# Kernel tuning notes

Measured on AMD Instinct MI355X. Metric: run time of the kernel, lower is better.

## Reference

```python
import jax, jax.numpy as jnp
import numpy as np

TOKENS, IN_F, OUT_F = 8192, 4096, 4096

def setup_inputs() -> dict:
    key = jax.random.key(0)
    k1, k2, k3, k4 = jax.random.split(key, 4)
    x = jax.random.randint(k1, (TOKENS, IN_F), -128, 128, dtype=jnp.int32).astype(jnp.int8)
    weight = jax.random.randint(k2, (OUT_F, IN_F), -128, 128, dtype=jnp.int32).astype(jnp.int8)
    # per-output-channel static dequant scale (small positive values, as for int8 quant)
    dequant_scale = (jax.random.uniform(k3, (OUT_F,), dtype=jnp.float32) * 0.01 + 1e-4)
    bias = (jax.random.normal(k4, (OUT_F,), dtype=jnp.float32) * 0.02).astype(jnp.float16)
    return {"x": x, "weight": weight, "dequant_scale": dequant_scale, "bias": bias}

def reference(x, weight, dequant_scale, bias):
    acc = jnp.matmul(x.astype(jnp.int32), weight.T.astype(jnp.int32))
    # fused epilogue: per-channel dequant + bias add, cast to fp16 output
    out = (acc.astype(jnp.float32) * dequant_scale[None, :]
           + bias.astype(jnp.float32)[None, :]).astype(jnp.float16)
    # module's forward returns (output, bias)
    return (out, bias)
```

## Files before the change

### kernel.cpp

```cpp
#include <hip/hip_runtime.h>
#include <hip/hip_fp16.h>

#define TOKENS 8192
#define IN_F   4096
#define OUT_F  4096
#define NKT    (IN_F / 64)

typedef __attribute__((ext_vector_type(4))) int i32x4;

__global__ void prep_kernel(const int4* __restrict__ xs, const int4* __restrict__ ws,
                            const float* __restrict__ bias,
                            int4* __restrict__ xp, int4* __restrict__ wp,
                            float* __restrict__ out_tail) {
    const int NX = TOKENS * IN_F / 16;
    const int NW = OUT_F * IN_F / 16;
    const int gid = blockIdx.x * blockDim.x + threadIdx.x;
    const int stride = gridDim.x * blockDim.x;
    for (int i = gid; i < NX + NW; i += stride) {
        const int4* s; int4* d; int j;
        if (i < NX) { s = xs; d = xp; j = i; }
        else        { s = ws; d = wp; j = i - NX; }
        int4 a = s[4 * j + 0];
        int4 b = s[4 * j + 1];
        int4 c = s[4 * j + 2];
        int4 e = s[4 * j + 3];
        int4 o;
        o.x = (int)((a.x & 0xffu) | ((a.y & 0xffu) << 8) | ((a.z & 0xffu) << 16) | ((a.w & 0xffu) << 24));
        o.y = (int)((b.x & 0xffu) | ((b.y & 0xffu) << 8) | ((b.z & 0xffu) << 16) | ((b.w & 0xffu) << 24));
        o.z = (int)((c.x & 0xffu) | ((c.y & 0xffu) << 8) | ((c.z & 0xffu) << 16) | ((c.w & 0xffu) << 24));
        o.w = (int)((e.x & 0xffu) | ((e.y & 0xffu) << 8) | ((e.z & 0xffu) << 16) | ((e.w & 0xffu) << 24));
        d[j] = o;
    }
    if (gid < OUT_F) out_tail[gid] = bias[gid];
}

__global__ __launch_bounds__(512, 2) void gemm_i8_kernel(
    const char* __restrict__ A,
    const char* __restrict__ B,
    const float* __restrict__ scale,
    const float* __restrict__ bias,
    float* __restrict__ out)
{
    __shared__ char lds[4][2][16384];

    const int tid  = threadIdx.x;
    const int wid  = tid >> 6;
    const int lane = tid & 63;
    const int wm   = wid >> 2;
    const int wn   = wid & 3;

    const int nwg = gridDim.x;
    const int bid = blockIdx.x;
    const int swz = (bid & 7) * (nwg >> 3) + (bid >> 3);
    const int tm = swz >> 4;
    const int tn = swz & 15;

    const char* ag = A + (size_t)(tm * 256) * IN_F;
    const char* bg = B + (size_t)(tn * 256) * IN_F;

    const int srow16 = wid * 16 + (lane >> 2);
    const int schunk = ((lane & 3) ^ ((lane >> 2) & 3)) << 4;
    const int ldst   = wid * 1024 + lane * 16;

    i32x4 acc[8][4];
#pragma unroll
    for (int m = 0; m < 8; ++m)
#pragma unroll
        for (int n = 0; n < 4; ++n)
            acc[m][n] = (i32x4){0, 0, 0, 0};

#define STAGE(r, t)                                                                        \
    do {                                                                                   \
        _Pragma("unroll")                                                                  \
        for (int j = 0; j < 2; ++j) {                                                      \
            size_t go = (size_t)(j * 128 + srow16) * IN_F + (size_t)(t) * 64 + schunk;     \
            __builtin_amdgcn_global_load_lds(                                              \
                (const __attribute__((address_space(1))) void*)(ag + go),                  \
                (__attribute__((address_space(3))) void*)(&lds[r][0][j * 8192 + ldst]),    \
                16, 0, 0);                                                                 \
            __builtin_amdgcn_global_load_lds(                                              \
                (const __attribute__((address_space(1))) void*)(bg + go),                  \
                (__attribute__((address_space(3))) void*)(&lds[r][1][j * 8192 + ldst]),    \
                16, 0, 0);                                                                 \
        }                                                                                  \
    } while (0)

    const int kg   = lane >> 4;
    const int sxa  = lane & 3;
    const int aoff = (wm * 128 + (lane & 15)) * 64 + ((kg ^ sxa) << 4);
    const int boff = (wn * 64  + (lane & 15)) * 64 + ((kg ^ sxa) << 4);

#define STEP(t, VM, DOSTAGE)                                                               \
    do {                                                                                   \
        asm volatile("s_waitcnt vmcnt(" #VM ")" ::: "memory");                             \
        __builtin_amdgcn_s_barrier();                                                      \
        asm volatile("" ::: "memory");                                                     \
        __builtin_amdgcn_sched_barrier(0);                                                 \
        if (DOSTAGE) STAGE(((t) + 3) & 3, (t) + 3);                                        \
        const char* al = &lds[(t) & 3][0][0];                                              \
        const char* bl = &lds[(t) & 3][1][0];                                              \
        i32x4 afr[8], bfr[4];                                                              \
        _Pragma("unroll")                                                                  \
        for (int m = 0; m < 8; ++m) afr[m] = *(const i32x4*)(al + aoff + m * 1024);        \
        _Pragma("unroll")                                                                  \
        for (int n = 0; n < 4; ++n) bfr[n] = *(const i32x4*)(bl + boff + n * 1024);        \
        __builtin_amdgcn_s_setprio(1);                                                     \
        _Pragma("unroll")                                                                  \
        for (int m = 0; m < 8; ++m)                                                        \
            _Pragma("unroll")                                                              \
            for (int n = 0; n < 4; ++n)                                                    \
                acc[m][n] = __builtin_amdgcn_mfma_i32_16x16x64_i8(                         \
                    afr[m], bfr[n], acc[m][n], 0, 0, 0);                                   \
        __builtin_amdgcn_s_setprio(0);                                                     \
    } while (0)

    STAGE(0, 0);
    STAGE(1, 1);
    STAGE(2, 2);

    for (int t = 0; t < NKT - 3; ++t) STEP(t, 8, 1);
    STEP(NKT - 3, 8, 0);
    STEP(NKT - 2, 4, 0);
    STEP(NKT - 1, 0, 0);

    const int col  = tn * 256 + wn * 64 + (lane & 15);
    const int row0 = tm * 256 + wm * 128 + ((lane >> 4) << 2);
    float sc[4], bi[4];
#pragma unroll
    for (int n = 0; n < 4; ++n) {
        sc[n] = scale[col + n * 16];
        bi[n] = bias[col + n * 16];
    }
#pragma unroll
    for (int m = 0; m < 8; ++m)
#pragma unroll
        for (int n = 0; n < 4; ++n)
#pragma unroll
            for (int r = 0; r < 4; ++r) {
                float v = (float)acc[m][n][r] * sc[n] + bi[n];
                out[(size_t)(row0 + m * 16 + r) * OUT_F + col + n * 16] =
                    (float)__float2half_rn(v);
            }
#undef STAGE
#undef STEP
}

extern "C" void kernel_launch(void* const* d_in, const int* in_sizes, int n_in,
                              void* d_out, int out_size, void* d_ws, size_t ws_size,
                              hipStream_t stream) {
    const int*   x_i32 = (const int*)d_in[0];
    const int*   w_i32 = (const int*)d_in[1];
    const float* scale = (const float*)d_in[2];
    const float* bias  = (const float*)d_in[3];
    float*       out   = (float*)d_out;

    char* xp = (char*)d_ws;
    char* wp = xp + (size_t)TOKENS * IN_F;

    prep_kernel<<<3072, 256, 0, stream>>>((const int4*)x_i32, (const int4*)w_i32, bias,
                                          (int4*)xp, (int4*)wp, out + (size_t)TOKENS * OUT_F);

    gemm_i8_kernel<<<(TOKENS / 256) * (OUT_F / 256), 512, 0, stream>>>(xp, wp, scale, bias, out);
}
```

Measured before the change: 192.0 us.

## Switch GEMM to 128x256 tiles with K=128 triple-buffered two-phase pipeline

The block tile shrinks from 256x256 to 128x256 while the K step grows from 64 to 128, and the LDS ring goes from four buffers to three. Each K tile is split into two phases, and the async global-to-LDS loads for tile t+2 are interleaved into those phases with explicit vmcnt waits and extra barriers. The grid doubles and per-thread accumulators halve, which should improve occupancy and load balance. In exchange, arithmetic intensity per block drops and more barriers are taken per K step.

```diff
diff --git a/kernel.cpp b/kernel.cpp
--- a/kernel.cpp
+++ b/kernel.cpp
@@ -4,8 +4,11 @@
 #define TOKENS 8192
 #define IN_F   4096
 #define OUT_F  4096
-#define NKT    (IN_F / 64)
+#define NKT    (IN_F / 128)
 
+#define ABYTES 16384
+#define BBYTES 32768
+#define BUFSZ  (ABYTES + BBYTES)
 typedef __attribute__((ext_vector_type(4))) int i32x4;
 
 __global__ void prep_kernel(const int4* __restrict__ xs, const int4* __restrict__ ws,
@@ -41,7 +44,7 @@
     const float* __restrict__ bias,
     float* __restrict__ out)
 {
-    __shared__ char lds[4][2][16384];
+    __shared__ char lds[3 * BUFSZ];
 
     const int tid  = threadIdx.x;
     const int wid  = tid >> 6;
@@ -55,76 +58,98 @@
     const int tm = swz >> 4;
     const int tn = swz & 15;
 
-    const char* ag = A + (size_t)(tm * 256) * IN_F;
+    const char* ag = A + (size_t)(tm * 128) * IN_F;
     const char* bg = B + (size_t)(tn * 256) * IN_F;
 
-    const int srow16 = wid * 16 + (lane >> 2);
-    const int schunk = ((lane & 3) ^ ((lane >> 2) & 3)) << 4;
-    const int ldst   = wid * 1024 + lane * 16;
+    const int schunk = ((tid & 7) ^ ((tid >> 3) & 7)) << 4;
+    const int srow   = tid >> 3;
+    const int ldst   = tid * 16;
 
-    i32x4 acc[8][4];
+#define STAGE_A(r, t, j)                                                                   \
+    __builtin_amdgcn_global_load_lds(                                                      \
+        (const __attribute__((address_space(1))) void*)(ag +                               \
+            (size_t)((j) * 64 + srow) * IN_F + (t) * 128 + schunk),                        \
+        (__attribute__((address_space(3))) void*)(&lds[(r) * BUFSZ + (j) * 8192 + ldst]),  \
+        16, 0, 0)
+
+#define STAGE_B(r, t, j)                                                                   \
+    __builtin_amdgcn_global_load_lds(                                                      \
+        (const __attribute__((address_space(1))) void*)(bg +                               \
+            (size_t)((j) * 64 + srow) * IN_F + (t) * 128 + schunk),                        \
+        (__attribute__((address_space(3))) void*)(&lds[(r) * BUFSZ + ABYTES +              \
+                                                       (j) * 8192 + ldst]),                \
+        16, 0, 0)
+
+    const int arow  = (wm * 64 + (lane & 15)) * 128;
+    const int brow  = (wn * 64 + (lane & 15)) * 128;
+    const int aswz0 = (((lane >> 4) ^ (lane & 7)) << 4);
+
+    i32x4 acc[4][4];
 #pragma unroll
-    for (int m = 0; m < 8; ++m)
+    for (int m = 0; m < 4; ++m)
 #pragma unroll
         for (int n = 0; n < 4; ++n)
             acc[m][n] = (i32x4){0, 0, 0, 0};
 
-#define STAGE(r, t)                                                                        \
+#define PHASE(r, t, kk, STAGES, TAILSYNC)                                                  \
     do {                                                                                   \
+        const char* Lr = &lds[(r) * BUFSZ];                                                \
+        const int swk = aswz0 ^ ((kk) << 6);                                               \
+        i32x4 afr[4], bfr[4];                                                              \
         _Pragma("unroll")                                                                  \
-        for (int j = 0; j < 2; ++j) {                                                      \
-            size_t go = (size_t)(j * 128 + srow16) * IN_F + (size_t)(t) * 64 + schunk;     \
-            __builtin_amdgcn_global_load_lds(                                              \
-                (const __attribute__((address_space(1))) void*)(ag + go),                  \
-                (__attribute__((address_space(3))) void*)(&lds[r][0][j * 8192 + ldst]),    \
-                16, 0, 0);                                                                 \
-            __builtin_amdgcn_global_load_lds(                                              \
-                (const __attribute__((address_space(1))) void*)(bg + go),                  \
-                (__attribute__((address_space(3))) void*)(&lds[r][1][j * 8192 + ldst]),    \
-                16, 0, 0);                                                                 \
-        }                                                                                  \
-    } while (0)
-
-    const int kg   = lane >> 4;
-    const int sxa  = lane & 3;
-    const int aoff = (wm * 128 + (lane & 15)) * 64 + ((kg ^ sxa) << 4);
-    const int boff = (wn * 64  + (lane & 15)) * 64 + ((kg ^ sxa) << 4);
-
-#define STEP(t, VM, DOSTAGE)                                                               \
-    do {                                                                                   \
-        asm volatile("s_waitcnt vmcnt(" #VM ")" ::: "memory");                             \
+        for (int m = 0; m < 4; ++m)                                                        \
+            afr[m] = *(const i32x4*)(Lr + arow + m * 2048 + swk);                          \
+        _Pragma("unroll")                                                                  \
+        for (int n = 0; n < 4; ++n)                                                        \
+            bfr[n] = *(const i32x4*)(Lr + ABYTES + brow + n * 2048 + swk);                 \
+        STAGES;                                                                            \
         __builtin_amdgcn_s_barrier();                                                      \
-        asm volatile("" ::: "memory");                                                     \
+        asm volatile("s_waitcnt lgkmcnt(0)" ::: "memory");                                 \
         __builtin_amdgcn_sched_barrier(0);                                                 \
-        if (DOSTAGE) STAGE(((t) + 3) & 3, (t) + 3);                                        \
-        const char* al = &lds[(t) & 3][0][0];                                              \
-        const char* bl = &lds[(t) & 3][1][0];                                              \
-        i32x4 afr[8], bfr[4];                                                              \
-        _Pragma("unroll")                                                                  \
-        for (int m = 0; m < 8; ++m) afr[m] = *(const i32x4*)(al + aoff + m * 1024);        \
-        _Pragma("unroll")                                                                  \
-        for (int n = 0; n < 4; ++n) bfr[n] = *(const i32x4*)(bl + boff + n * 1024);        \
         __builtin_amdgcn_s_setprio(1);                                                     \
         _Pragma("unroll")                                                                  \
-        for (int m = 0; m < 8; ++m)                                                        \
+        for (int m = 0; m < 4; ++m)                                                        \
             _Pragma("unroll")                                                              \
             for (int n = 0; n < 4; ++n)                                                    \
                 acc[m][n] = __builtin_amdgcn_mfma_i32_16x16x64_i8(                         \
                     afr[m], bfr[n], acc[m][n], 0, 0, 0);                                   \
         __builtin_amdgcn_s_setprio(0);                                                     \
+        TAILSYNC;                                                                          \
+        __builtin_amdgcn_s_barrier();                                                      \
+        __builtin_amdgcn_sched_barrier(0);                                                 \
     } while (0)
 
-    STAGE(0, 0);
-    STAGE(1, 1);
-    STAGE(2, 2);
+#define VM6 asm volatile("s_waitcnt vmcnt(6)" ::: "memory")
+#define VM0 asm volatile("s_waitcnt vmcnt(0)" ::: "memory")
 
-    for (int t = 0; t < NKT - 3; ++t) STEP(t, 8, 1);
-    STEP(NKT - 3, 8, 0);
-    STEP(NKT - 2, 4, 0);
-    STEP(NKT - 1, 0, 0);
+#define TILE_FULL(t, r, rs)                                                                \
+    do {                                                                                   \
+        PHASE(r, t, 0, { STAGE_A(rs, (t) + 2, 0); STAGE_A(rs, (t) + 2, 1);                 \
+                         STAGE_B(rs, (t) + 2, 0); }, );                                    \
+        PHASE(r, t, 1, { STAGE_B(rs, (t) + 2, 1); STAGE_B(rs, (t) + 2, 2);                 \
+                         STAGE_B(rs, (t) + 2, 3); }, VM6);                                 \
+    } while (0)
+
+    STAGE_A(0, 0, 0); STAGE_A(0, 0, 1);
+    STAGE_B(0, 0, 0); STAGE_B(0, 0, 1); STAGE_B(0, 0, 2); STAGE_B(0, 0, 3);
+    STAGE_A(1, 1, 0); STAGE_A(1, 1, 1);
+    STAGE_B(1, 1, 0); STAGE_B(1, 1, 1); STAGE_B(1, 1, 2); STAGE_B(1, 1, 3);
+    VM6;
+    __builtin_amdgcn_s_barrier();
+    __builtin_amdgcn_sched_barrier(0);
+
+    for (int tt = 0; tt < 30; tt += 3) {
+        TILE_FULL(tt + 0, 0, 2);
+        TILE_FULL(tt + 1, 1, 0);
+        TILE_FULL(tt + 2, 2, 1);
+    }
+    PHASE(0, 30, 0, , );
+    PHASE(0, 30, 1, , VM0);
+    PHASE(1, 31, 0, , );
+    PHASE(1, 31, 1, , );
 
     const int col  = tn * 256 + wn * 64 + (lane & 15);
-    const int row0 = tm * 256 + wm * 128 + ((lane >> 4) << 2);
+    const int row0 = tm * 128 + wm * 64 + ((lane >> 4) << 2);
     float sc[4], bi[4];
 #pragma unroll
     for (int n = 0; n < 4; ++n) {
@@ -132,7 +157,7 @@
         bi[n] = bias[col + n * 16];
     }
 #pragma unroll
-    for (int m = 0; m < 8; ++m)
+    for (int m = 0; m < 4; ++m)
 #pragma unroll
         for (int n = 0; n < 4; ++n)
 #pragma unroll
@@ -141,8 +166,12 @@
                 out[(size_t)(row0 + m * 16 + r) * OUT_F + col + n * 16] =
                     (float)__float2half_rn(v);
             }
-#undef STAGE
-#undef STEP
+#undef STAGE_A
+#undef STAGE_B
+#undef PHASE
+#undef TILE_FULL
+#undef VM6
+#undef VM0
 }
 
 extern "C" void kernel_launch(void* const* d_in, const int* in_sizes, int n_in,
@@ -160,5 +189,5 @@
     prep_kernel<<<3072, 256, 0, stream>>>((const int4*)x_i32, (const int4*)w_i32, bias,
                                           (int4*)xp, (int4*)wp, out + (size_t)TOKENS * OUT_F);
 
-    gemm_i8_kernel<<<(TOKENS / 256) * (OUT_F / 256), 512, 0, stream>>>(xp, wp, scale, bias, out);
+    gemm_i8_kernel<<<(TOKENS / 128) * (OUT_F / 256), 512, 0, stream>>>(xp, wp, scale, bias, out);
 }
```

Result: no change. 195.1 us (+1.6%).

## Switch to K=128 double-buffered LDS pipeline with split fragment loads

Applied to the files above, without the earlier changes.

The K-tile grows from 64 to 128 bytes and the 4-stage ring of small buffers becomes a double buffer of 64KB stages, which halves the number of barriers per K. Within each tile the second half's A fragments are loaded from LDS while the first half's MFMAs run, and the next tile's global-to-LDS copies are issued mid-tile. The trade-off is a shallower prefetch (one tile ahead) that waits for all loads at the end of each tile, so global latency may be exposed more often. The swizzle changes to an 8-chunk XOR to match the 128-byte rows.

```diff
diff --git a/kernel.cpp b/kernel.cpp
--- a/kernel.cpp
+++ b/kernel.cpp
@@ -4,8 +4,11 @@
 #define TOKENS 8192
 #define IN_F   4096
 #define OUT_F  4096
-#define NKT    (IN_F / 64)
+#define NKT    (IN_F / 128)
 
+#define ABYTES 32768
+#define BBYTES 32768
+#define BUFSZ  (ABYTES + BBYTES)
 typedef __attribute__((ext_vector_type(4))) int i32x4;
 
 __global__ void prep_kernel(const int4* __restrict__ xs, const int4* __restrict__ ws,
@@ -41,7 +44,7 @@
     const float* __restrict__ bias,
     float* __restrict__ out)
 {
-    __shared__ char lds[4][2][16384];
+    __shared__ char lds[2 * BUFSZ];
 
     const int tid  = threadIdx.x;
     const int wid  = tid >> 6;
@@ -58,9 +61,31 @@
     const char* ag = A + (size_t)(tm * 256) * IN_F;
     const char* bg = B + (size_t)(tn * 256) * IN_F;
 
-    const int srow16 = wid * 16 + (lane >> 2);
-    const int schunk = ((lane & 3) ^ ((lane >> 2) & 3)) << 4;
-    const int ldst   = wid * 1024 + lane * 16;
+    const int schunk = ((tid & 7) ^ ((tid >> 3) & 7)) << 4;
+    const int srow   = tid >> 3;
+    const int ldst   = tid * 16;
+
+#define STAGE(r, t)                                                                        \
+    do {                                                                                   \
+        _Pragma("unroll")                                                                  \
+        for (int j = 0; j < 4; ++j) {                                                      \
+            size_t go = (size_t)(j * 64 + srow) * IN_F + (size_t)(t) * 128 + schunk;       \
+            __builtin_amdgcn_global_load_lds(                                              \
+                (const __attribute__((address_space(1))) void*)(ag + go),                  \
+                (__attribute__((address_space(3))) void*)(&lds[(r) * BUFSZ +               \
+                                                              j * 8192 + ldst]),           \
+                16, 0, 0);                                                                 \
+            __builtin_amdgcn_global_load_lds(                                              \
+                (const __attribute__((address_space(1))) void*)(bg + go),                  \
+                (__attribute__((address_space(3))) void*)(&lds[(r) * BUFSZ + ABYTES +      \
+                                                              j * 8192 + ldst]),           \
+                16, 0, 0);                                                                 \
+        }                                                                                  \
+    } while (0)
+
+    const int arow = (wm * 128 + (lane & 15)) * 128;
+    const int brow = (wn * 64  + (lane & 15)) * 128;
+    const int sw0  = ((lane >> 4) ^ (lane & 7)) << 4;
 
     i32x4 acc[8][4];
 #pragma unroll
@@ -69,59 +94,56 @@
         for (int n = 0; n < 4; ++n)
             acc[m][n] = (i32x4){0, 0, 0, 0};
 
-#define STAGE(r, t)                                                                        \
+    STAGE(0, 0);
+    asm volatile("s_waitcnt vmcnt(0)" ::: "memory");
+    __builtin_amdgcn_s_barrier();
+    __builtin_amdgcn_sched_barrier(0);
+
+#define TILE(t, DOSTAGE)                                                                   \
     do {                                                                                   \
+        const char* Lr = &lds[((t) & 1) * BUFSZ];                                          \
+        i32x4 af0[8], bf0[4], bf1[4];                                                      \
         _Pragma("unroll")                                                                  \
-        for (int j = 0; j < 2; ++j) {                                                      \
-            size_t go = (size_t)(j * 128 + srow16) * IN_F + (size_t)(t) * 64 + schunk;     \
-            __builtin_amdgcn_global_load_lds(                                              \
-                (const __attribute__((address_space(1))) void*)(ag + go),                  \
-                (__attribute__((address_space(3))) void*)(&lds[r][0][j * 8192 + ldst]),    \
-                16, 0, 0);                                                                 \
-            __builtin_amdgcn_global_load_lds(                                              \
-                (const __attribute__((address_space(1))) void*)(bg + go),                  \
-                (__attribute__((address_space(3))) void*)(&lds[r][1][j * 8192 + ldst]),    \
-                16, 0, 0);                                                                 \
-        }                                                                                  \
-    } while (0)
-
-    const int kg   = lane >> 4;
-    const int sxa  = lane & 3;
-    const int aoff = (wm * 128 + (lane & 15)) * 64 + ((kg ^ sxa) << 4);
-    const int boff = (wn * 64  + (lane & 15)) * 64 + ((kg ^ sxa) << 4);
-
-#define STEP(t, VM, DOSTAGE)                                                               \
-    do {                                                                                   \
-        asm volatile("s_waitcnt vmcnt(" #VM ")" ::: "memory");                             \
-        __builtin_amdgcn_s_barrier();                                                      \
-        asm volatile("" ::: "memory");                                                     \
+        for (int m = 0; m < 8; ++m)                                                        \
+            af0[m] = *(const i32x4*)(Lr + arow + m * 2048 + sw0);                          \
+        _Pragma("unroll")                                                                  \
+        for (int n = 0; n < 4; ++n)                                                        \
+            bf0[n] = *(const i32x4*)(Lr + ABYTES + brow + n * 2048 + sw0);                 \
+        _Pragma("unroll")                                                                  \
+        for (int n = 0; n < 4; ++n)                                                        \
+            bf1[n] = *(const i32x4*)(Lr + ABYTES + brow + n * 2048 + (sw0 ^ 0x40));        \
+        if (DOSTAGE) STAGE(((t) + 1) & 1, (t) + 1);                                        \
+        asm volatile("s_waitcnt lgkmcnt(4)" ::: "memory");                                 \
         __builtin_amdgcn_sched_barrier(0);                                                 \
-        if (DOSTAGE) STAGE(((t) + 3) & 3, (t) + 3);                                        \
-        const char* al = &lds[(t) & 3][0][0];                                              \
-        const char* bl = &lds[(t) & 3][1][0];                                              \
-        i32x4 afr[8], bfr[4];                                                              \
-        _Pragma("unroll")                                                                  \
-        for (int m = 0; m < 8; ++m) afr[m] = *(const i32x4*)(al + aoff + m * 1024);        \
-        _Pragma("unroll")                                                                  \
-        for (int n = 0; n < 4; ++n) bfr[n] = *(const i32x4*)(bl + boff + n * 1024);        \
         __builtin_amdgcn_s_setprio(1);                                                     \
         _Pragma("unroll")                                                                  \
         for (int m = 0; m < 8; ++m)                                                        \
             _Pragma("unroll")                                                              \
             for (int n = 0; n < 4; ++n)                                                    \
                 acc[m][n] = __builtin_amdgcn_mfma_i32_16x16x64_i8(                         \
-                    afr[m], bfr[n], acc[m][n], 0, 0, 0);                                   \
+                    af0[m], bf0[n], acc[m][n], 0, 0, 0);                                   \
         __builtin_amdgcn_s_setprio(0);                                                     \
+        i32x4 af1[8];                                                                      \
+        _Pragma("unroll")                                                                  \
+        for (int m = 0; m < 8; ++m)                                                        \
+            af1[m] = *(const i32x4*)(Lr + arow + m * 2048 + (sw0 ^ 0x40));                 \
+        asm volatile("s_waitcnt lgkmcnt(0)" ::: "memory");                                 \
+        __builtin_amdgcn_sched_barrier(0);                                                 \
+        __builtin_amdgcn_s_setprio(1);                                                     \
+        _Pragma("unroll")                                                                  \
+        for (int m = 0; m < 8; ++m)                                                        \
+            _Pragma("unroll")                                                              \
+            for (int n = 0; n < 4; ++n)                                                    \
+                acc[m][n] = __builtin_amdgcn_mfma_i32_16x16x64_i8(                         \
+                    af1[m], bf1[n], acc[m][n], 0, 0, 0);                                   \
+        __builtin_amdgcn_s_setprio(0);                                                     \
+        asm volatile("s_waitcnt vmcnt(0)" ::: "memory");                                   \
+        __builtin_amdgcn_s_barrier();                                                      \
+        __builtin_amdgcn_sched_barrier(0);                                                 \
     } while (0)
 
-    STAGE(0, 0);
-    STAGE(1, 1);
-    STAGE(2, 2);
-
-    for (int t = 0; t < NKT - 3; ++t) STEP(t, 8, 1);
-    STEP(NKT - 3, 8, 0);
-    STEP(NKT - 2, 4, 0);
-    STEP(NKT - 1, 0, 0);
+    for (int t = 0; t < NKT - 1; ++t) TILE(t, 1);
+    TILE(NKT - 1, 0);
 
     const int col  = tn * 256 + wn * 64 + (lane & 15);
     const int row0 = tm * 256 + wm * 128 + ((lane >> 4) << 2);
@@ -142,7 +164,7 @@
                     (float)__float2half_rn(v);
             }
 #undef STAGE
-#undef STEP
+#undef TILE
 }
 
 extern "C" void kernel_launch(void* const* d_in, const int* in_sizes, int n_in,
```

After: 177.0 us. -7.8%, faster.

## Rework LDS tile layout, XCD-aware tile swizzle, and issue prefetch after fragment reads

Applied to the files above, without the earlier changes.

Changes the LDS staging layout so each pair of rows is interleaved into 128-byte lines, replacing the XOR swizzle with a paired-row layout and adjusting the fragment read offsets to match. The block-to-tile mapping is reworked so each XCD handles a compact 8x4 rectangle of output tiles, aiming for better L2 reuse of A and B panels. The next-stage global-to-LDS prefetch is now issued after the LDS fragment reads rather than before them. Together these target LDS bank conflicts, cache locality and load ordering, at the risk of new bank conflicts if the paired-row layout does not spread lanes evenly across banks.

```diff
diff --git a/kernel.cpp b/kernel.cpp
--- a/kernel.cpp
+++ b/kernel.cpp
@@ -4,8 +4,10 @@
 #define TOKENS 8192
 #define IN_F   4096
 #define OUT_F  4096
-#define NKT    (IN_F / 64)
+#define NK64   (IN_F / 64)
 
+#define REG    16384
+#define BUFSZ  (2 * REG)
 typedef __attribute__((ext_vector_type(4))) int i32x4;
 
 __global__ void prep_kernel(const int4* __restrict__ xs, const int4* __restrict__ ws,
@@ -41,7 +43,7 @@
     const float* __restrict__ bias,
     float* __restrict__ out)
 {
-    __shared__ char lds[4][2][16384];
+    __shared__ char lds[4 * BUFSZ];
 
     const int tid  = threadIdx.x;
     const int wid  = tid >> 6;
@@ -49,18 +51,43 @@
     const int wm   = wid >> 2;
     const int wn   = wid & 3;
 
-    const int nwg = gridDim.x;
-    const int bid = blockIdx.x;
-    const int swz = (bid & 7) * (nwg >> 3) + (bid >> 3);
-    const int tm = swz >> 4;
-    const int tn = swz & 15;
+    const int bid   = blockIdx.x;
+    const int xcd   = bid & 7;
+    const int j9    = bid >> 3;
+    const int rect  = (j9 >> 5) * 8 + xcd;
+    const int jj    = j9 & 31;
+    const int tm    = (rect & 3) * 8 + (jj & 7);
+    const int tn    = (rect >> 2) * 4 + (jj >> 3);
 
     const char* ag = A + (size_t)(tm * 256) * IN_F;
     const char* bg = B + (size_t)(tn * 256) * IN_F;
 
-    const int srow16 = wid * 16 + (lane >> 2);
-    const int schunk = ((lane & 3) ^ ((lane >> 2) & 3)) << 4;
-    const int ldst   = wid * 1024 + lane * 16;
+    const int  srow_a = (wid * 16) + ((lane >> 3) * 2) + ((lane >> 2) & 1);
+    const size_t gsub = (size_t)srow_a * IN_F + (lane & 3) * 16;
+    const int  ldst   = tid * 16;
+
+#define STAGE(r, t)                                                                        \
+    do {                                                                                   \
+        _Pragma("unroll")                                                                  \
+        for (int i = 0; i < 2; ++i) {                                                      \
+            size_t go = (size_t)(i * 128) * IN_F + gsub + (size_t)(t) * 64;                \
+            __builtin_amdgcn_global_load_lds(                                              \
+                (const __attribute__((address_space(1))) void*)(ag + go),                  \
+                (__attribute__((address_space(3))) void*)(&lds[(r) * BUFSZ +               \
+                                                              i * 8192 + ldst]),           \
+                16, 0, 0);                                                                 \
+            __builtin_amdgcn_global_load_lds(                                              \
+                (const __attribute__((address_space(1))) void*)(bg + go),                  \
+                (__attribute__((address_space(3))) void*)(&lds[(r) * BUFSZ + REG +         \
+                                                              i * 8192 + ldst]),           \
+                16, 0, 0);                                                                 \
+        }                                                                                  \
+    } while (0)
+
+    const int low  = lane & 15;
+    const int hi   = lane >> 4;
+    const int aoff = (wm * 64 + (low >> 1)) * 128 + (((low & 1) * 4 + hi) << 4);
+    const int boff = (wn * 32 + (low >> 1)) * 128 + (((low & 1) * 4 + hi) << 4);
 
     i32x4 acc[8][4];
 #pragma unroll
@@ -69,59 +96,42 @@
         for (int n = 0; n < 4; ++n)
             acc[m][n] = (i32x4){0, 0, 0, 0};
 
-#define STAGE(r, t)                                                                        \
-    do {                                                                                   \
-        _Pragma("unroll")                                                                  \
-        for (int j = 0; j < 2; ++j) {                                                      \
-            size_t go = (size_t)(j * 128 + srow16) * IN_F + (size_t)(t) * 64 + schunk;     \
-            __builtin_amdgcn_global_load_lds(                                              \
-                (const __attribute__((address_space(1))) void*)(ag + go),                  \
-                (__attribute__((address_space(3))) void*)(&lds[r][0][j * 8192 + ldst]),    \
-                16, 0, 0);                                                                 \
-            __builtin_amdgcn_global_load_lds(                                              \
-                (const __attribute__((address_space(1))) void*)(bg + go),                  \
-                (__attribute__((address_space(3))) void*)(&lds[r][1][j * 8192 + ldst]),    \
-                16, 0, 0);                                                                 \
-        }                                                                                  \
-    } while (0)
+    STAGE(0, 0);
+    STAGE(1, 1);
+    STAGE(2, 2);
 
-    const int kg   = lane >> 4;
-    const int sxa  = lane & 3;
-    const int aoff = (wm * 128 + (lane & 15)) * 64 + ((kg ^ sxa) << 4);
-    const int boff = (wn * 64  + (lane & 15)) * 64 + ((kg ^ sxa) << 4);
-
-#define STEP(t, VM, DOSTAGE)                                                               \
+#define TILE(t, VM, DOSTAGE)                                                               \
     do {                                                                                   \
         asm volatile("s_waitcnt vmcnt(" #VM ")" ::: "memory");                             \
         __builtin_amdgcn_s_barrier();                                                      \
-        asm volatile("" ::: "memory");                                                     \
         __builtin_amdgcn_sched_barrier(0);                                                 \
+        const char* Lr = &lds[((t) & 3) * BUFSZ];                                          \
+        i32x4 af[8], bf[4];                                                                \
+        _Pragma("unroll")                                                                  \
+        for (int n = 0; n < 4; ++n)                                                        \
+            bf[n] = *(const i32x4*)(Lr + REG + boff + n * 1024);                           \
+        _Pragma("unroll")                                                                  \
+        for (int m = 0; m < 4; ++m)                                                        \
+            af[m] = *(const i32x4*)(Lr + aoff + m * 1024);                                 \
+        _Pragma("unroll")                                                                  \
+        for (int m = 4; m < 8; ++m)                                                        \
+            af[m] = *(const i32x4*)(Lr + aoff + m * 1024);                                 \
         if (DOSTAGE) STAGE(((t) + 3) & 3, (t) + 3);                                        \
-        const char* al = &lds[(t) & 3][0][0];                                              \
-        const char* bl = &lds[(t) & 3][1][0];                                              \
-        i32x4 afr[8], bfr[4];                                                              \
-        _Pragma("unroll")                                                                  \
-        for (int m = 0; m < 8; ++m) afr[m] = *(const i32x4*)(al + aoff + m * 1024);        \
-        _Pragma("unroll")                                                                  \
-        for (int n = 0; n < 4; ++n) bfr[n] = *(const i32x4*)(bl + boff + n * 1024);        \
         __builtin_amdgcn_s_setprio(1);                                                     \
         _Pragma("unroll")                                                                  \
         for (int m = 0; m < 8; ++m)                                                        \
             _Pragma("unroll")                                                              \
             for (int n = 0; n < 4; ++n)                                                    \
                 acc[m][n] = __builtin_amdgcn_mfma_i32_16x16x64_i8(                         \
-                    afr[m], bfr[n], acc[m][n], 0, 0, 0);                                   \
+                    af[m], bf[n], acc[m][n], 0, 0, 0);                                     \
         __builtin_amdgcn_s_setprio(0);                                                     \
     } while (0)
 
-    STAGE(0, 0);
-    STAGE(1, 1);
-    STAGE(2, 2);
-
-    for (int t = 0; t < NKT - 3; ++t) STEP(t, 8, 1);
-    STEP(NKT - 3, 8, 0);
-    STEP(NKT - 2, 4, 0);
-    STEP(NKT - 1, 0, 0);
+#pragma unroll 1
+    for (int t = 0; t <= NK64 - 4; ++t) TILE(t, 8, 1);
+    TILE(NK64 - 3, 8, 0);
+    TILE(NK64 - 2, 4, 0);
+    TILE(NK64 - 1, 0, 0);
 
     const int col  = tn * 256 + wn * 64 + (lane & 15);
     const int row0 = tm * 256 + wm * 128 + ((lane >> 4) << 2);
@@ -142,7 +152,7 @@
                     (float)__float2half_rn(v);
             }
 #undef STAGE
-#undef STEP
+#undef TILE
 }
 
 extern "C" void kernel_launch(void* const* d_in, const int* in_sizes, int n_in,
```

Result: no change. 189.4 us (-1.3%).
